# Kernel optimization log

Measured on AMD Instinct MI355X. Metric: run time of the kernel, lower is better.

Reference implementation:

```python
import jax, jax.numpy as jnp
import numpy as np

C, H, D = 64, 2, 32
NQ, NA, NE, F_IN = 8192, 32768, 500000, 128
E_E2Q, E_E2E, E_E2A, E_Q2A = 131072, 800000, 262144, 32768
N_POS, N_NEG = 8192, 24576
# node types: 0=question, 1=answer, 2=entity
# edge types (src_type, dst_type): e2q=(2,0), e2e=(2,2), e2a=(2,1), q2a=(0,1)
REL_ST = [(2, 0), (2, 2), (2, 1), (0, 1)]


def _edges(k, n_src, n_dst, e):
    k1, k2 = jax.random.split(k)
    return jnp.stack([jax.random.randint(k1, (e,), 0, n_src),
                      jax.random.randint(k2, (e,), 0, n_dst)]).astype(jnp.int32)


def setup_inputs():
    key = jax.random.key(0)
    ks = jax.random.split(key, 16)
    inp = {
        'x_question': jax.random.normal(ks[0], (NQ, F_IN), jnp.float32),
        'x_answer': jax.random.normal(ks[1], (NA, F_IN), jnp.float32),
        'x_entity': jax.random.normal(ks[2], (NE, F_IN), jnp.float32),
        'e_e2q': _edges(ks[3], NE, NQ, E_E2Q),
        'e_e2e': _edges(ks[4], NE, NE, E_E2E),
        'e_e2a': _edges(ks[5], NE, NA, E_E2A),
        'e_q2a': _edges(ks[6], NQ, NA, E_Q2A),
        'pos_idx': _edges(ks[7], NQ, NA, N_POS),
        'neg_idx': _edges(ks[8], NQ, NA, N_NEG),
        # learned parameters (stacked over the 3 node types / 4 edge types)
        'W_in': jax.random.normal(ks[9], (3, F_IN, C), jnp.float32) / np.sqrt(F_IN).astype(np.float32),
        'b_in': jnp.zeros((3, C), jnp.float32),
        'bn_gamma': jnp.ones((3, C), jnp.float32),
        'bn_beta': jnp.zeros((3, C), jnp.float32),
        'W_kqv': jax.random.normal(ks[10], (3, C, 3 * C), jnp.float32) / np.sqrt(C).astype(np.float32),
        'b_kqv': jnp.zeros((3, 3 * C), jnp.float32),
        'A_k': jax.random.normal(ks[11], (4, H, D, D), jnp.float32) / np.sqrt(D).astype(np.float32),
        'A_v': jax.random.normal(ks[12], (4, H, D, D), jnp.float32) / np.sqrt(D).astype(np.float32),
        'p_rel': jnp.ones((4, H), jnp.float32),
        'W_out': jax.random.normal(ks[13], (3, C, C), jnp.float32) / np.sqrt(C).astype(np.float32),
        'b_out': jnp.zeros((3, C), jnp.float32),
        'skip': jnp.ones((3,), jnp.float32),
    }
    return inp


def _segment_attn(scores, vals, dst, n):
    # scores [E,H], vals [E,H,D]: softmax over incoming edges per dst node, weighted scatter-add
    m = jax.ops.segment_max(scores, dst, num_segments=n)          # [N,H]
    e = jnp.exp(scores - m[dst])                                   # [E,H]
    s = jax.ops.segment_sum(e, dst, num_segments=n)                # [N,H]
    w = e / s[dst]
    return jax.ops.segment_sum(vals * w[..., None], dst, num_segments=n)  # [N,H,D]


def _forward(x_question, x_answer, x_entity, W_in, b_in, bn_gamma, bn_beta,
             W_kqv, b_kqv, A_k, A_v, p_rel, W_out, b_out, skip, edges):
    xs = [x_question, x_answer, x_entity]
    h = []
    for t in range(3):
        y = jax.nn.relu(xs[t] @ W_in[t] + b_in[t])
        mu = y.mean(0)
        var = y.var(0)  # biased, as in torch BN training mode
        y = bn_gamma[t] * (y - mu) * jax.lax.rsqrt(var + 1e-5) + bn_beta[t]
        h.append(y)
    kqv = [h[t] @ W_kqv[t] + b_kqv[t] for t in range(3)]
    k = [kv[:, :C].reshape(-1, H, D) for kv in kqv]
    q = [kv[:, C:2 * C].reshape(-1, H, D) for kv in kqv]
    v = [kv[:, 2 * C:].reshape(-1, H, D) for kv in kqv]
    by_dst = {0: [], 1: [], 2: []}
    inv_sqrt_d = jnp.float32(1.0 / np.sqrt(D))
    for r, ((st, dt), ei) in enumerate(zip(REL_ST, edges)):
        src, dst = ei[0], ei[1]
        k_r = jnp.einsum('ehd,hdf->ehf', k[st][src], A_k[r])   # per-relation key transform
        v_r = jnp.einsum('ehd,hdf->ehf', v[st][src], A_v[r])   # per-relation value transform
        sc = (q[dt][dst] * k_r).sum(-1) * p_rel[r] * inv_sqrt_d  # [E,H]
        by_dst[dt].append((sc, v_r, dst))
    out = []
    for t in range(3):
        sc = jnp.concatenate([a for a, _, _ in by_dst[t]], axis=0)
        vr = jnp.concatenate([b for _, b, _ in by_dst[t]], axis=0)
        dst = jnp.concatenate([c for _, _, c in by_dst[t]], axis=0)
        n = h[t].shape[0]
        agg = _segment_attn(sc, vr, dst, n).reshape(n, C)
        a = jax.nn.gelu(agg, approximate=False) @ W_out[t] + b_out[t]
        g = jax.nn.sigmoid(skip[t])
        out.append(g * a + (1.0 - g) * h[t])
    return out  # [z_question, z_answer, z_entity]


def reference(x_question, x_answer, x_entity, e_e2q, e_e2e, e_e2a, e_q2a,
              pos_idx, neg_idx, W_in, b_in, bn_gamma, bn_beta, W_kqv, b_kqv,
              A_k, A_v, p_rel, W_out, b_out, skip):
    zq, za, ze = _forward(x_question, x_answer, x_entity, W_in, b_in, bn_gamma,
                          bn_beta, W_kqv, b_kqv, A_k, A_v, p_rel, W_out, b_out,
                          skip, [e_e2q, e_e2e, e_e2a, e_q2a])
    pos_pred = (zq[pos_idx[0]] * za[pos_idx[1]]).sum(-1)
    neg_pred = (zq[neg_idx[0]] * za[neg_idx[1]]).sum(-1)
    return pos_pred, neg_pred, zq, za, ze
```

## Files before the change

kernel.cpp:

```cpp
#include <hip/hip_runtime.h>
#include <hip/hip_bf16.h>
#include <hip/hip_fp16.h>
#include <math.h>

#define NQ 8192
#define NA 32768
#define NE 500000
#define F_IN 128
#define E_E2Q 131072
#define E_E2E 800000
#define E_E2A 262144
#define E_Q2A 32768
#define N_POS 8192
#define N_NEG 24576

#define NT_TOTAL (NQ + NA + NE)
#define E_TOTAL (E_E2Q + E_E2E + E_E2A + E_Q2A)
#define NBLK_SCAN ((NT_TOTAL + 1023) / 1024)
#define CDIV(a, b) (((a) + (b) - 1) / (b))

#define BASE_Q 0
#define BASE_A NQ
#define BASE_E (NQ + NA)

#define GIN_Q 128
#define GIN_A 512
#define GIN_E 768

#define GB_Q 2048
#define GB_E 4096
#define GB_A 8192

#define TOP_Q 64
#define TOP_A 256
#define TOP_E 3907

typedef _Float16 half8_t __attribute__((ext_vector_type(8)));
typedef _Float16 half4_t __attribute__((ext_vector_type(4)));
typedef _Float16 half2_t __attribute__((ext_vector_type(2)));
typedef float f32x4_t __attribute__((ext_vector_type(4)));

__device__ inline void load_lds16(const void* g, void* l) {
  __builtin_amdgcn_global_load_lds((const __attribute__((address_space(1))) void*)g,
                                   (__attribute__((address_space(3))) void*)l, 16, 0, 0);
}

__device__ inline float fast_gelu(float v) {
  float u = 1.5957691216057308f * fmaf(0.044715f * v * v, v, v);
  return v / (1.f + __expf(-u));
}


__global__ __launch_bounds__(256) void prep_misc(
    float* __restrict__ row_start_f,
    const float* __restrict__ W_in, _Float16* __restrict__ WinT,
    const float* __restrict__ W_out, _Float16* __restrict__ WoutT)
{
  int bid = blockIdx.x;
  if (bid < 128) {
    size_t i = (size_t)bid * 256 + threadIdx.x;
    size_t stride = (size_t)128 * 256;
    for (; i < NT_TOTAL; i += stride) row_start_f[i] = 0.f;
  } else if (bid < 320) {
    int b = bid - 128;
    int t = b >> 6, n = b & 63, k = threadIdx.x;
    if (k < 136) {
      float v = (k < 128) ? W_in[(size_t)t * 128 * 64 + (size_t)k * 64 + n] : 0.f;
      WinT[((size_t)t * 64 + n) * 136 + k] = (_Float16)v;
    }
  } else {
    int b = bid - 320;
    int t = b >> 6, n = b & 63, k = threadIdx.x;
    if (k < 72) {
      float v = (k < 64) ? W_out[(size_t)t * 64 * 64 + (size_t)k * 64 + n] : 0.f;
      WoutT[((size_t)t * 64 + n) * 72 + k] = (_Float16)v;
    }
  }
}


__global__ __launch_bounds__(256) void gemm_inproj_all(
    const float* __restrict__ xq, const float* __restrict__ xa,
    const float* __restrict__ xe,
    const _Float16* __restrict__ WinT, const float* __restrict__ b_in,
    _Float16* __restrict__ y_h, float* __restrict__ bstats)
{
  __shared__ __align__(16) float bufA[32 * 128];
  __shared__ __align__(16) float bufB[32 * 128];
  __shared__ _Float16 Bs[64 * 136];
  __shared__ float s1[64], s2[64];

  int bid = blockIdx.x;
  int t, lb, nb;
  const float* Af;
  _Float16* oh;
  if (bid < GIN_Q)              { t = 0; lb = bid;                 nb = GIN_Q; Af = xq; oh = y_h; }
  else if (bid < GIN_Q + GIN_A) { t = 1; lb = bid - GIN_Q;         nb = GIN_A; Af = xa; oh = y_h + (size_t)NQ * 64; }
  else                          { t = 2; lb = bid - GIN_Q - GIN_A; nb = GIN_E; Af = xe; oh = y_h + (size_t)(NQ + NA) * 64; }
  int M = (t == 0) ? NQ : (t == 1) ? NA : NE;
  int nh = CDIV(M, 32);
  const _Float16* WT = WinT + (size_t)t * 64 * 136;
  const float* bias = b_in + t * 64;

  int tid = threadIdx.x, w = tid >> 6, l = tid & 63;
  int lr = l & 15, lg = l >> 4;
  int wrow = (w & 1) * 16;
  int wcol = (w >> 1) * 32;

  for (int idx = tid; idx < 64 * 136 / 8; idx += 256)
    *(half8_t*)&Bs[idx * 8] = *(const half8_t*)&WT[(size_t)idx * 8];
  if (tid < 64) { s1[tid] = 0.f; s2[tid] = 0.f; }

  float bval[2];
  bval[0] = bias[wcol + lr];
  bval[1] = bias[wcol + 16 + lr];
// ... 58 lines not shown
        oh[(size_t)row * 64 + col] = (_Float16)val;
        ps1[ct] += val;
        ps2[ct] += val * val;
      }
    }
    __builtin_amdgcn_s_barrier();
    float* tmp = cur; cur = nxt; nxt = tmp;
  }

#pragma unroll
  for (int ct = 0; ct < 2; ++ct) {
    int col = wcol + ct * 16 + lr;
    atomicAdd(&s1[col], ps1[ct]);
    atomicAdd(&s2[col], ps2[ct]);
  }
  __syncthreads();
  if (tid < 64) {
    bstats[(size_t)blockIdx.x * 128 + tid] = s1[tid];
    bstats[(size_t)blockIdx.x * 128 + 64 + tid] = s2[tid];
  }
}


__global__ __launch_bounds__(256) void gemm_out_all(
    const _Float16* __restrict__ agg_h, const _Float16* __restrict__ y_h,
    const _Float16* __restrict__ WoutT, const float* __restrict__ b_out,
    const float* __restrict__ scale, const float* __restrict__ shift,
    const float* __restrict__ skip, float* __restrict__ zout)
{
  __shared__ _Float16 Bs[64 * 72];
  int bid = blockIdx.x;
  int t, row0, M;
  size_t nodeoff;
  if (bid < TOP_Q)              { t = 0; row0 = bid * 128;              M = NQ; nodeoff = 0; }
  else if (bid < TOP_Q + TOP_A) { t = 1; row0 = (bid - TOP_Q) * 128;    M = NA; nodeoff = NQ; }
  else                          { t = 2; row0 = (bid - TOP_Q - TOP_A) * 128; M = NE; nodeoff = NQ + NA; }
  const _Float16* Ah = agg_h + nodeoff * 64;
  const _Float16* resh = y_h + nodeoff * 64;
  float* Cf = zout + nodeoff * 64;
  const _Float16* WT = WoutT + (size_t)t * 64 * 72;
  const float* bias = b_out + t * 64;
  const float* rsc = scale + t * 64;
  const float* rsh = shift + t * 64;

  int tid = threadIdx.x;
  int w = tid >> 6, l = tid & 63;
  int lr = l & 15, lg = l >> 4;

  for (int idx = tid; idx < 64 * 72 / 8; idx += 256)
    *(half8_t*)&Bs[idx * 8] = *(const half8_t*)&WT[(size_t)idx * 8];

  half8_t afrag[2][2];
#pragma unroll
  for (int rt = 0; rt < 2; ++rt) {
    int gr = row0 + w * 32 + rt * 16 + lr;
    bool ok = gr < M;
#pragma unroll
    for (int ks = 0; ks < 2; ++ks) {
      half8_t h8 = {};
      if (ok) h8 = *(const half8_t*)&Ah[(size_t)gr * 64 + ks * 32 + lg * 8];
      afrag[rt][ks] = h8;
    }
  }
  __syncthreads();

  f32x4_t acc[2][4] = {};
#pragma unroll
  for (int ks = 0; ks < 2; ++ks) {
#pragma unroll
    for (int ct = 0; ct < 4; ++ct) {
      half8_t b = *(const half8_t*)&Bs[(ct * 16 + lr) * 72 + ks * 32 + lg * 8];
      acc[0][ct] = __builtin_amdgcn_mfma_f32_16x16x32_f16(afrag[0][ks], b, acc[0][ct], 0, 0, 0);
      acc[1][ct] = __builtin_amdgcn_mfma_f32_16x16x32_f16(afrag[1][ks], b, acc[1][ct], 0, 0, 0);
    }
  }

  float g = 1.f / (1.f + __expf(-skip[t]));
  float gb = 1.f - g;
#pragma unroll
  for (int rt = 0; rt < 2; ++rt) {
    int rbase = row0 + w * 32 + rt * 16 + lg * 4;
#pragma unroll
    for (int ct = 0; ct < 4; ++ct) {
      int col = ct * 16 + lr;
      float bval = bias[col];
#pragma unroll
      for (int j = 0; j < 4; ++j) {
        int row = rbase + j;
        if (row >= M) continue;
        float val = acc[rt][ct][j] + bval;
        float rv = (float)resh[(size_t)row * 64 + col];
        Cf[(size_t)row * 64 + col] = g * val + gb * (rsc[col] * rv + rsh[col]);
      }
    }
  }
}


template <int BM, int BNT, int KTOT>
__global__ __launch_bounds__(BM * 2) void gemm_mfma(
    const _Float16* __restrict__ Ah,
    const _Float16* __restrict__ WT, const float* __restrict__ bias, int M,
    _Float16* __restrict__ oh, int LDO)
{
  constexpr int KP = KTOT + 8;
  constexpr int NTHR = BM * 2;
  constexpr int TP = BNT + 8;
  constexpr int SZ_AB = (BM * KP + BNT * KP) * 2;
  constexpr int SZ_T = 128 * TP * 2;
  constexpr int SZ = SZ_AB > SZ_T ? SZ_AB : SZ_T;
  __shared__ __align__(16) char smem[SZ];
  _Float16* As = (_Float16*)smem;
  _Float16* Bs = As + BM * KP;
  _Float16* Ts = (_Float16*)smem;
  int tid = threadIdx.x;
  int row0 = blockIdx.x * BM;
  int colbase = blockIdx.y * BNT;

  {
    constexpr int CH = KTOT / 8;
    for (int idx = tid; idx < BM * CH; idx += NTHR) {
      int row = idx / CH, c = idx % CH;
      int gr = row0 + row;
      half8_t a8 = {};
      if (gr < M) a8 = *(const half8_t*)&Ah[(size_t)gr * KTOT + c * 8];
      *(half8_t*)&As[row * KP + c * 8] = a8;
    }
  }
  {
    const _Float16* wsrc = WT + (size_t)colbase * KP;
    for (int idx = tid; idx < BNT * KP / 8; idx += NTHR)
      *(half8_t*)&Bs[idx * 8] = *(const half8_t*)&wsrc[(size_t)idx * 8];
  }
  __syncthreads();

  int w = tid >> 6, l = tid & 63;
  int lr = l & 15, lg = l >> 4;
  constexpr int NCT = BNT / 16;
  constexpr int NKS = KTOT / 32;
  f32x4_t acc[2][NCT] = {};
#pragma unroll
  for (int ks = 0; ks < NKS; ++ks) {
    half8_t a0 = *(const half8_t*)&As[(w * 32 + lr) * KP + ks * 32 + lg * 8];
    half8_t a1 = *(const half8_t*)&As[(w * 32 + 16 + lr) * KP + ks * 32 + lg * 8];
#pragma unroll
    for (int ct = 0; ct < NCT; ++ct) {
      half8_t b = *(const half8_t*)&Bs[(ct * 16 + lr) * KP + ks * 32 + lg * 8];
      acc[0][ct] = __builtin_amdgcn_mfma_f32_16x16x32_f16(a0, b, acc[0][ct], 0, 0, 0);
      acc[1][ct] = __builtin_amdgcn_mfma_f32_16x16x32_f16(a1, b, acc[1][ct], 0, 0, 0);
    }
  }

  float bval[NCT];
#pragma unroll
  for (int ct = 0; ct < NCT; ++ct) bval[ct] = bias[colbase + ct * 16 + lr];

#pragma unroll
  for (int rt = 0; rt < 2; ++rt) {
    __syncthreads();
    int r2base = w * 16 + lg * 4;
#pragma unroll
    for (int ct = 0; ct < NCT; ++ct) {
      int colL = ct * 16 + lr;
#pragma unroll
      for (int j = 0; j < 4; ++j)
        Ts[(r2base + j) * TP + colL] = (_Float16)(acc[rt][ct][j] + bval[ct]);
    }
    __syncthreads();
    constexpr int C8 = BNT / 8;
    for (int idx = tid; idx < 128 * C8; idx += NTHR) {
      int r2 = idx / C8, c8 = (idx % C8) * 8;
      int gr = row0 + (r2 >> 4) * 32 + rt * 16 + (r2 & 15);
      if (gr < M)
        *(half8_t*)&oh[(size_t)gr * LDO + colbase + c8] = *(const half8_t*)&Ts[r2 * TP + c8];
    }
  }
}


__global__ __launch_bounds__(256) void stats_reduce(const float* __restrict__ bstats,
                                                    float* __restrict__ stats) {
  __shared__ float sh[256];
  int t = blockIdx.x >> 7;
  int c = blockIdx.x & 127;
  int nb = (t == 0) ? GIN_Q : (t == 1) ? GIN_A : GIN_E;
  int base = (t == 0) ? 0 : (t == 1) ? GIN_Q : (GIN_Q + GIN_A);
  float s = 0.f;
  for (int i = threadIdx.x; i < nb; i += 256)
    s += bstats[(size_t)(base + i) * 128 + c];
  sh[threadIdx.x] = s;
  __syncthreads();
  for (int off2 = 128; off2 > 0; off2 >>= 1) {
    if (threadIdx.x < off2) sh[threadIdx.x] += sh[threadIdx.x + off2];
    __syncthreads();
  }
  if (threadIdx.x == 0) stats[t * 128 + c] = sh[0];
}

__global__ void bn_finalize(const float* __restrict__ stats,
                            const float* __restrict__ gamma, const float* __restrict__ beta,
                            float* __restrict__ scale, float* __restrict__ shift) {
  int t = threadIdx.x;
  if (t >= 192) return;
  int ty = t >> 6, c = t & 63;
  float invN = (ty == 0) ? (1.f / NQ) : (ty == 1) ? (1.f / NA) : (1.f / NE);
  float mu = stats[ty * 128 + c] * invN;
  float var = stats[ty * 128 + 64 + c] * invN - mu * mu;
  float rs = rsqrtf(var + 1e-5f);
  float gm = gamma[ty * 64 + c];
  scale[t] = gm * rs;
  shift[t] = beta[ty * 64 + c] - gm * mu * rs;
}

__global__ void kqv_bias2(const float* __restrict__ b_kqv, const float* __restrict__ W_kqv,
                          const float* __restrict__ shift, float* __restrict__ bias2) {
  int t = blockIdx.x, n = threadIdx.x;
  float s = b_kqv[t * 192 + n];
  for (int k = 0; k < 64; ++k)
    s += shift[t * 64 + k] * W_kqv[(size_t)t * 64 * 192 + k * 192 + n];
  bias2[t * 192 + n] = s;
}


__global__ void wprep_kqv(const float* __restrict__ W_kqv, const float* __restrict__ bias2,
                          const float* __restrict__ A_k, const float* __restrict__ A_v,
                          const float* __restrict__ scale,
                          _Float16* __restrict__ WqT, _Float16* __restrict__ WeT,
                          _Float16* __restrict__ WaT, float* __restrict__ bias_big) {
  int j = blockIdx.x;
  int c = threadIdx.x;
  int t, jj, bofs;
  _Float16* W;
  if (j < 192)      { t = 0; jj = j;       W = WqT; bofs = 0; }
  else if (j < 512) { t = 2; jj = j - 192; W = WeT; bofs = 192; }
  else              { t = 1; jj = j - 512; W = WaT; bofs = 512; }
  const float* Wt = W_kqv + (size_t)t * 64 * 192;
  const float* b2 = bias2 + t * 192;
  int mode = 0, rel = 0, sub = 0;
  if (t == 1) { mode = 1; rel = (jj < 64) ? 2 : 3; sub = jj & 63; }
  else if (jj >= 64 && jj < 128) { mode = 1; rel = (t == 0) ? 0 : 1; sub = jj - 64; }
  else if (jj >= 128) {
    mode = 2; sub = (jj - 128) & 63;
    rel = (t == 0) ? 3 : ((jj - 128) >> 6);
  }
  int h = sub >> 5, x = sub & 31;
  float wv, bv;
  if (mode == 0) {
    wv = Wt[(size_t)c * 192 + jj];
    bv = b2[jj];
  } else if (mode == 1) {
    const float* Ar = A_k + ((size_t)rel * 2048 + h * 1024 + x * 32);
    float s = 0.f, sb = 0.f;
    for (int f = 0; f < 32; ++f) {
      float a = Ar[f];
      s = fmaf(a, Wt[(size_t)c * 192 + 64 + h * 32 + f], s);
      sb = fmaf(a, b2[64 + h * 32 + f], sb);
    }
    wv = s; bv = sb;
  } else {
    const float* Ar = A_v + ((size_t)rel * 2048 + h * 1024 + x);
    float s = 0.f, sb = 0.f;
    for (int d = 0; d < 32; ++d) {
      float a = Ar[d * 32];
      s = fmaf(a, Wt[(size_t)c * 192 + 128 + h * 32 + d], s);
      sb = fmaf(a, b2[128 + h * 32 + d], sb);
    }
    wv = s; bv = sb;
  }
  wv *= scale[t * 64 + c];
  W[(size_t)jj * 72 + c] = (_Float16)wv;
  if (c < 8) W[(size_t)jj * 72 + 64 + c] = (_Float16)0.f;
  if (c == 0) bias_big[bofs + jj] = bv;
}


__global__ __launch_bounds__(256) void hist_all(
    const int* __restrict__ d0, const int* __restrict__ d1,
    const int* __restrict__ d2, const int* __restrict__ d3,
    unsigned* __restrict__ cnt)
{
  int i = blockIdx.x * blockDim.x + threadIdx.x;
  int stride = gridDim.x * blockDim.x;
  for (; i < E_TOTAL; i += stride) {
    if (i < E_E2Q) atomicAdd(&cnt[BASE_Q + d0[i]], 1u);
    else if (i < E_E2Q + E_E2E) atomicAdd(&cnt[BASE_E + d1[i - E_E2Q]], 1u);
    else if (i < E_E2Q + E_E2E + E_E2A) atomicAdd(&cnt[BASE_A + d2[i - E_E2Q - E_E2E]], 1u);
    else atomicAdd(&cnt[BASE_A + d3[i - E_E2Q - E_E2E - E_E2A]], 1u);
  }
}

__global__ __launch_bounds__(256) void scan1(unsigned* __restrict__ arr, int n,
                                             unsigned* __restrict__ bsums) {
  __shared__ unsigned sh[256];
  int t = threadIdx.x;
  int base = blockIdx.x * 1024 + t * 4;
  unsigned v[4];
  unsigned s = 0;
#pragma unroll
  for (int j = 0; j < 4; ++j) {
    v[j] = (base + j < n) ? arr[base + j] : 0u;
    s += v[j];
  }
  sh[t] = s;
  __syncthreads();
  for (int off = 1; off < 256; off <<= 1) {
    unsigned x = (t >= off) ? sh[t - off] : 0u;
    __syncthreads();
    sh[t] += x;
    __syncthreads();
  }
  unsigned run = sh[t] - s;
#pragma unroll
  for (int j = 0; j < 4; ++j) {
    if (base + j < n) arr[base + j] = run;
    run += v[j];
  }
  if (t == 255) bsums[blockIdx.x] = sh[255];
}

__global__ __launch_bounds__(256) void scan2(unsigned* __restrict__ bsums, int nb) {
  __shared__ unsigned sh[256];
  __shared__ unsigned carry;
  int t = threadIdx.x;
  if (t == 0) carry = 0;
  __syncthreads();
  for (int chunk = 0; chunk < nb; chunk += 256) {
    int i = chunk + t;
    unsigned v = (i < nb) ? bsums[i] : 0u;
    sh[t] = v;
    __syncthreads();
    for (int off = 1; off < 256; off <<= 1) {
      unsigned x = (t >= off) ? sh[t - off] : 0u;
      __syncthreads();
      sh[t] += x;
      __syncthreads();
    }
    unsigned inc = sh[t];
    unsigned c = carry;
    __syncthreads();
    if (i < nb) bsums[i] = c + inc - v;
    if (t == 255) carry = c + sh[255];
    __syncthreads();
  }
}

__global__ __launch_bounds__(256) void scan3(unsigned* __restrict__ arr,
                                             const unsigned* __restrict__ bsums,
                                             unsigned* __restrict__ cursor, int n) {
  int t = threadIdx.x;
  int base = blockIdx.x * 1024 + t * 4;
  unsigned add = bsums[blockIdx.x];
#pragma unroll
  for (int j = 0; j < 4; ++j) {
    int idx = base + j;
    if (idx < n) {
      unsigned r = arr[idx] + add;
      arr[idx] = r;
      cursor[idx] = r;
    }
  }
}

__global__ __launch_bounds__(256) void scatter_all(
    const int* __restrict__ s0, const int* __restrict__ d0,
    const int* __restrict__ s1, const int* __restrict__ d1,
    const int* __restrict__ s2, const int* __restrict__ d2,
    const int* __restrict__ s3, const int* __restrict__ d3,
    unsigned* __restrict__ cursor, unsigned* __restrict__ eidx)
{
  int i = blockIdx.x * blockDim.x + threadIdx.x;
  int stride = gridDim.x * blockDim.x;
  for (; i < E_TOTAL; i += stride) {
    unsigned pos, pay;
    if (i < E_E2Q) {
      pos = atomicAdd(&cursor[BASE_Q + d0[i]], 1u);
      pay = (unsigned)(s0[i] * 320);
    } else if (i < E_E2Q + E_E2E) {
      int k = i - E_E2Q;
      pos = atomicAdd(&cursor[BASE_E + d1[k]], 1u);
      pay = (unsigned)(s1[k] * 320);
    } else if (i < E_E2Q + E_E2E + E_E2A) {
      int k = i - E_E2Q - E_E2E;
      pos = atomicAdd(&cursor[BASE_A + d2[k]], 1u);
      pay = (unsigned)(s2[k] * 320);
    } else {
      int k = i - E_E2Q - E_E2E - E_E2A;
      pos = atomicAdd(&cursor[BASE_A + d3[k]], 1u);
      pay = (unsigned)(s3[k] * 192) | 0x80000000u;
    }
    eidx[pos] = pay;
  }
}


template <int NREL>
__device__ __forceinline__ void gather_body(
    int bidLocal, int nblocks, int N, int nodebase,
    const unsigned* __restrict__ row_start, const unsigned* __restrict__ row_end,
    const unsigned* __restrict__ eidx,
    const _Float16* __restrict__ baseA, int vofA,
    const _Float16* __restrict__ baseB, int vofB,
    const _Float16* __restrict__ qtA, int ldqA,
    const _Float16* __restrict__ qtB, int ldqB,
    const float* __restrict__ prelA, const float* __restrict__ prelB,
    _Float16* __restrict__ agg)
{
  int lane = threadIdx.x & 63;
  int h = lane >> 5, f = lane & 31;
  int idx2 = h * 32 + 2 * (f & 15);
  const float isd = 0.17677669529663687f;
  float pr0 = prelA[h] * isd;
  float pr1 = (NREL == 2) ? prelB[h] * isd : 0.f;

// ... 91 lines not shown
  }
}

__global__ __launch_bounds__(256) void gather_all(
    const unsigned* __restrict__ row_start, const unsigned* __restrict__ row_end,
    const unsigned* __restrict__ eidx,
    const _Float16* __restrict__ kqvQ, const _Float16* __restrict__ kqvE,
    const _Float16* __restrict__ kqvA,
    const float* __restrict__ p_rel, _Float16* __restrict__ agg)
{
  int bid = blockIdx.x;
  if (bid < GB_Q) {
    gather_body<1>(bid, GB_Q, NQ, BASE_Q, row_start, row_end, eidx,
                   kqvE, 128, kqvE, 128, kqvQ + 64, 192, kqvQ + 64, 192,
                   p_rel + 0, p_rel + 0, agg);
  } else if (bid < GB_Q + GB_E) {
    gather_body<1>(bid - GB_Q, GB_E, NE, BASE_E, row_start, row_end, eidx,
                   kqvE, 192, kqvE, 192, kqvE + 64, 320, kqvE + 64, 320,
                   p_rel + 2, p_rel + 2, agg);
  } else {
    gather_body<2>(bid - GB_Q - GB_E, GB_A, NA, BASE_A, row_start, row_end, eidx,
                   kqvE, 256, kqvQ, 128, kqvA, 128, kqvA + 64, 128,
                   p_rel + 4, p_rel + 6, agg);
  }
}


__global__ void pred_all(const int* __restrict__ pos, const int* __restrict__ neg,
                         const float* __restrict__ zq, const float* __restrict__ za,
                         float* __restrict__ outp) {
  int i = blockIdx.x * blockDim.x + threadIdx.x;
  if (i >= N_POS + N_NEG) return;
  int k; const int* qi; const int* ai; float* o;
  if (i < N_POS) { k = i; qi = pos; ai = pos + N_POS; o = outp; }
  else { k = i - N_POS; qi = neg; ai = neg + N_NEG; o = outp + N_POS; }
  const float4* a = (const float4*)(zq + (size_t)qi[k] * 64);
  const float4* b = (const float4*)(za + (size_t)ai[k] * 64);
  float ssum = 0.f;
#pragma unroll
  for (int j = 0; j < 16; ++j) {
    float4 x = a[j], y = b[j];
    ssum += x.x * y.x + x.y * y.y + x.z * y.z + x.w * y.w;
  }
  o[k] = ssum;
}

// ... 21 lines not shown
  const float* p_rel = (const float*)d_in[17];
  const float* W_out = (const float*)d_in[18];
  const float* b_out = (const float*)d_in[19];
  const float* skip = (const float*)d_in[20];
  float* out = (float*)d_out;

  float* ws = (float*)d_ws;
  size_t off = 0;
  _Float16* y_h = (_Float16*)(ws + off);    off += (size_t)NT_TOTAL * 32;
  _Float16* kqvQ = (_Float16*)(ws + off);   off += (size_t)NQ * 96;
  _Float16* kqvE = (_Float16*)(ws + off);   off += (size_t)NE * 160;
  _Float16* kqvA = (_Float16*)(ws + off);   off += (size_t)NA * 64;
  _Float16* agg_h = (_Float16*)(ws + off);  off += (size_t)NT_TOTAL * 32;
  float* stats = ws + off;                  off += 384;
  float* scale = ws + off;                  off += 192;
  float* shift = ws + off;                  off += 192;
  float* bias2 = ws + off;                  off += 576;
  float* bias_big = ws + off;               off += 640;
  _Float16* WqT = (_Float16*)(ws + off);    off += 192 * 72 / 2;
  _Float16* WeT = (_Float16*)(ws + off);    off += 320 * 72 / 2;
  _Float16* WaT = (_Float16*)(ws + off);    off += 128 * 72 / 2;
  _Float16* WinT = (_Float16*)(ws + off);   off += 3 * 64 * 136 / 2;
  _Float16* WoutT = (_Float16*)(ws + off);  off += 3 * 64 * 72 / 2;
  float* bstats = ws + off;                 off += (size_t)(GIN_Q + GIN_A + GIN_E) * 128;
  unsigned* row_start = (unsigned*)(ws + off); off += NT_TOTAL;
  unsigned* cursor = (unsigned*)(ws + off);    off += NT_TOTAL;
  unsigned* bsums = (unsigned*)(ws + off);     off += 1024;
  unsigned* eidx = (unsigned*)(ws + off);      off += E_TOTAL + 8;

  float* zq_out = out + (N_POS + N_NEG);

  prep_misc<<<dim3(512), dim3(256), 0, stream>>>((float*)row_start, W_in, WinT, W_out, WoutT);

  gemm_inproj_all<<<dim3(GIN_Q + GIN_A + GIN_E), dim3(256), 0, stream>>>(
      xq, xa, xe, WinT, b_in, y_h, bstats);

  stats_reduce<<<dim3(384), dim3(256), 0, stream>>>(bstats, stats);
  bn_finalize<<<dim3(1), dim3(192), 0, stream>>>(stats, bn_gamma, bn_beta, scale, shift);
  kqv_bias2<<<dim3(3), dim3(192), 0, stream>>>(b_kqv, W_kqv, shift, bias2);
  wprep_kqv<<<dim3(640), dim3(64), 0, stream>>>(W_kqv, bias2, A_k, A_v, scale,
                                                WqT, WeT, WaT, bias_big);

  gemm_mfma<256, 192, 64><<<dim3(CDIV(NQ, 256)), dim3(512), 0, stream>>>(
      y_h, WqT, bias_big, NQ, kqvQ, 192);
  gemm_mfma<256, 160, 64><<<dim3(CDIV(NE, 256), 2), dim3(512), 0, stream>>>(
      y_h + (size_t)(NQ + NA) * 64, WeT, bias_big + 192, NE, kqvE, 320);
  gemm_mfma<256, 128, 64><<<dim3(CDIV(NA, 256)), dim3(512), 0, stream>>>(
      y_h + (size_t)NQ * 64, WaT, bias_big + 512, NA, kqvA, 128);

  hist_all<<<dim3(2048), dim3(256), 0, stream>>>(
      e_e2q + E_E2Q, e_e2e + E_E2E, e_e2a + E_E2A, e_q2a + E_Q2A, row_start);
  scan1<<<dim3(NBLK_SCAN), dim3(256), 0, stream>>>(row_start, NT_TOTAL, bsums);
  scan2<<<dim3(1), dim3(256), 0, stream>>>(bsums, NBLK_SCAN);
  scan3<<<dim3(NBLK_SCAN), dim3(256), 0, stream>>>(row_start, bsums, cursor, NT_TOTAL);
  scatter_all<<<dim3(2048), dim3(256), 0, stream>>>(
      e_e2q, e_e2q + E_E2Q, e_e2e, e_e2e + E_E2E,
      e_e2a, e_e2a + E_E2A, e_q2a, e_q2a + E_Q2A, cursor, eidx);

  gather_all<<<dim3(GB_Q + GB_E + GB_A), dim3(256), 0, stream>>>(
      row_start, cursor, eidx, kqvQ, kqvE, kqvA, p_rel, agg_h);

  gemm_out_all<<<dim3(TOP_Q + TOP_A + TOP_E), dim3(256), 0, stream>>>(
      agg_h, y_h, WoutT, b_out, scale, shift, skip, zq_out);

  pred_all<<<dim3(CDIV(N_POS + N_NEG, 256)), dim3(256), 0, stream>>>(
      pos_idx, neg_idx, zq_out, zq_out + (size_t)NQ * 64, out);
}
```

Before: 709.7 us.

## Merge independent launches into horizontally fused kernels to cut launch count

Horizontally fuses independent stages into shared launches, with block ranges selecting the work. The edge histogram rides with the input projection, the BN stats reduction with scan1, BN finalize and bias2 with scan2, and weight prep with scan3. The three KQV GEMMs and the CSR scatter now share one launch with dynamic shared memory. This removes many small launches and serial gaps so that graph-building work overlaps the dense GEMMs. In exchange, the fused kernels carry a larger shared-memory footprint and 512-thread blocks for the scatter part, which may lower occupancy.

New measurement: 655.1 us. 1.08x faster.

```diff
diff --git a/kernel.cpp b/kernel.cpp
--- a/kernel.cpp
+++ b/kernel.cpp
@@ -26,6 +26,8 @@
 #define GIN_Q 128
 #define GIN_A 512
 #define GIN_E 768
+#define GIN_TOT (GIN_Q + GIN_A + GIN_E)
+#define HB 1024
 
 #define GB_Q 2048
 #define GB_E 4096
@@ -35,8 +37,14 @@
 #define TOP_A 256
 #define TOP_E 3907
 
+#define KQ_Q 32
+#define KQ_E 1954
+#define KQ_A 128
+#define KQ_TOT (KQ_Q + 2 * KQ_E + KQ_A)
+#define SCB 2048
+#define SMEM_KQV 64512
+
 typedef _Float16 half8_t __attribute__((ext_vector_type(8)));
-typedef _Float16 half4_t __attribute__((ext_vector_type(4)));
 typedef _Float16 half2_t __attribute__((ext_vector_type(2)));
 typedef float f32x4_t __attribute__((ext_vector_type(4)));
 
@@ -79,11 +87,14 @@
 }
 
 
-__global__ __launch_bounds__(256) void gemm_inproj_all(
+__global__ __launch_bounds__(256) void inproj_hist_all(
     const float* __restrict__ xq, const float* __restrict__ xa,
     const float* __restrict__ xe,
     const _Float16* __restrict__ WinT, const float* __restrict__ b_in,
-    _Float16* __restrict__ y_h, float* __restrict__ bstats)
+    _Float16* __restrict__ y_h, float* __restrict__ bstats,
+    const int* __restrict__ hd0, const int* __restrict__ hd1,
+    const int* __restrict__ hd2, const int* __restrict__ hd3,
+    unsigned* __restrict__ cnt)
 {
   __shared__ __align__(16) float bufA[32 * 128];
   __shared__ __align__(16) float bufB[32 * 128];
@@ -91,6 +102,19 @@
   __shared__ float s1[64], s2[64];
 
   int bid = blockIdx.x;
+  if (bid >= GIN_TOT) {
+    int i = (bid - GIN_TOT) * 256 + threadIdx.x;
+    int stride = HB * 256;
+    for (; i < E_TOTAL; i += stride) {
+      if (i < E_E2Q) atomicAdd(&cnt[BASE_Q + hd0[i]], 1u);
+      else if (i < E_E2Q + E_E2E) atomicAdd(&cnt[BASE_E + hd1[i - E_E2Q]], 1u);
+      else if (i < E_E2Q + E_E2E + E_E2A)
+        atomicAdd(&cnt[BASE_A + hd2[i - E_E2Q - E_E2E]], 1u);
+      else atomicAdd(&cnt[BASE_A + hd3[i - E_E2Q - E_E2E - E_E2A]], 1u);
+    }
+    return;
+  }
+
   int t, lb, nb;
   const float* Af;
   _Float16* oh;
@@ -195,213 +219,145 @@
 }
 
 
-__global__ __launch_bounds__(256) void gemm_out_all(
-    const _Float16* __restrict__ agg_h, const _Float16* __restrict__ y_h,
-    const _Float16* __restrict__ WoutT, const float* __restrict__ b_out,
-    const float* __restrict__ scale, const float* __restrict__ shift,
-    const float* __restrict__ skip, float* __restrict__ zout)
-{
-  __shared__ _Float16 Bs[64 * 72];
+__global__ __launch_bounds__(256) void reduce_scan1(
+    const float* __restrict__ bstats, float* __restrict__ stats,
+    unsigned* __restrict__ arr, unsigned* __restrict__ bsums)
+{
+  __shared__ __align__(16) char shbuf[1024];
   int bid = blockIdx.x;
-  int t, row0, M;
-  size_t nodeoff;
-  if (bid < TOP_Q)              { t = 0; row0 = bid * 128;              M = NQ; nodeoff = 0; }
-  else if (bid < TOP_Q + TOP_A) { t = 1; row0 = (bid - TOP_Q) * 128;    M = NA; nodeoff = NQ; }
-  else                          { t = 2; row0 = (bid - TOP_Q - TOP_A) * 128; M = NE; nodeoff = NQ + NA; }
-  const _Float16* Ah = agg_h + nodeoff * 64;
-  const _Float16* resh = y_h + nodeoff * 64;
-  float* Cf = zout + nodeoff * 64;
-  const _Float16* WT = WoutT + (size_t)t * 64 * 72;
-  const float* bias = b_out + t * 64;
-  const float* rsc = scale + t * 64;
-  const float* rsh = shift + t * 64;
-
-  int tid = threadIdx.x;
-  int w = tid >> 6, l = tid & 63;
-  int lr = l & 15, lg = l >> 4;
-
-  for (int idx = tid; idx < 64 * 72 / 8; idx += 256)
-    *(half8_t*)&Bs[idx * 8] = *(const half8_t*)&WT[(size_t)idx * 8];
-
-  half8_t afrag[2][2];
-#pragma unroll
-  for (int rt = 0; rt < 2; ++rt) {
-    int gr = row0 + w * 32 + rt * 16 + lr;
-    bool ok = gr < M;
-#pragma unroll
-    for (int ks = 0; ks < 2; ++ks) {
-      half8_t h8 = {};
-      if (ok) h8 = *(const half8_t*)&Ah[(size_t)gr * 64 + ks * 32 + lg * 8];
-      afrag[rt][ks] = h8;
-    }
-  }
-  __syncthreads();
-
-  f32x4_t acc[2][4] = {};
-#pragma unroll
-  for (int ks = 0; ks < 2; ++ks) {
-#pragma unroll
-    for (int ct = 0; ct < 4; ++ct) {
-      half8_t b = *(const half8_t*)&Bs[(ct * 16 + lr) * 72 + ks * 32 + lg * 8];
-      acc[0][ct] = __builtin_amdgcn_mfma_f32_16x16x32_f16(afrag[0][ks], b, acc[0][ct], 0, 0, 0);
-      acc[1][ct] = __builtin_amdgcn_mfma_f32_16x16x32_f16(afrag[1][ks], b, acc[1][ct], 0, 0, 0);
-    }
-  }
-
-  float g = 1.f / (1.f + __expf(-skip[t]));
-  float gb = 1.f - g;
-#pragma unroll
-  for (int rt = 0; rt < 2; ++rt) {
-    int rbase = row0 + w * 32 + rt * 16 + lg * 4;
-#pragma unroll
-    for (int ct = 0; ct < 4; ++ct) {
-      int col = ct * 16 + lr;
-      float bval = bias[col];
-#pragma unroll
-      for (int j = 0; j < 4; ++j) {
-        int row = rbase + j;
-        if (row >= M) continue;
-        float val = acc[rt][ct][j] + bval;
-        float rv = (float)resh[(size_t)row * 64 + col];
-        Cf[(size_t)row * 64 + col] = g * val + gb * (rsc[col] * rv + rsh[col]);
+  int t0 = threadIdx.x;
+  if (bid < 384) {
+    float* sh = (float*)shbuf;
+    int t = bid >> 7, c = bid & 127;
+    int nb = (t == 0) ? GIN_Q : (t == 1) ? GIN_A : GIN_E;
+    int base = (t == 0) ? 0 : (t == 1) ? GIN_Q : (GIN_Q + GIN_A);
+    float s = 0.f;
+    for (int i = t0; i < nb; i += 256)
+      s += bstats[(size_t)(base + i) * 128 + c];
+    sh[t0] = s;
+    __syncthreads();
+    for (int off2 = 128; off2 > 0; off2 >>= 1) {
+      if (t0 < off2) sh[t0] += sh[t0 + off2];
+      __syncthreads();
+    }
+    if (t0 == 0) stats[t * 128 + c] = sh[0];
+  } else {
+    unsigned* sh = (unsigned*)shbuf;
+    int blk = bid - 384;
+    int base = blk * 1024 + t0 * 4;
+    unsigned v[4];
+    unsigned s = 0;
+#pragma unroll
+    for (int j = 0; j < 4; ++j) {
+      v[j] = (base + j < NT_TOTAL) ? arr[base + j] : 0u;
+      s += v[j];
+    }
+    sh[t0] = s;
+    __syncthreads();
+    for (int off = 1; off < 256; off <<= 1) {
+      unsigned x = (t0 >= off) ? sh[t0 - off] : 0u;
+      __syncthreads();
+      sh[t0] += x;
+      __syncthreads();
+    }
+    unsigned run = sh[t0] - s;
+#pragma unroll
+    for (int j = 0; j < 4; ++j) {
+      if (base + j < NT_TOTAL) arr[base + j] = run;
+      run += v[j];
+    }
+    if (t0 == 255) bsums[blk] = sh[255];
+  }
+}
+
+
+__global__ __launch_bounds__(256) void scan2_bn(
+    unsigned* __restrict__ bsums, int nbk,
+    const float* __restrict__ stats,
+    const float* __restrict__ gamma, const float* __restrict__ beta,
+    float* __restrict__ scale, float* __restrict__ shift,
+    const float* __restrict__ b_kqv, const float* __restrict__ W_kqv,
+    float* __restrict__ bias2)
+{
+  int t0 = threadIdx.x;
+  if (blockIdx.x == 0) {
+    __shared__ unsigned sh[256];
+    __shared__ unsigned carry;
+    if (t0 == 0) carry = 0;
+    __syncthreads();
+    for (int chunk = 0; chunk < nbk; chunk += 256) {
+      int i = chunk + t0;
+      unsigned v = (i < nbk) ? bsums[i] : 0u;
+      sh[t0] = v;
+      __syncthreads();
+      for (int off = 1; off < 256; off <<= 1) {
+        unsigned x = (t0 >= off) ? sh[t0 - off] : 0u;
+        __syncthreads();
+        sh[t0] += x;
+        __syncthreads();
       }
-    }
-  }
-}
-
-
-template <int BM, int BNT, int KTOT>
-__global__ __launch_bounds__(BM * 2) void gemm_mfma(
-    const _Float16* __restrict__ Ah,
-    const _Float16* __restrict__ WT, const float* __restrict__ bias, int M,
-    _Float16* __restrict__ oh, int LDO)
-{
-  constexpr int KP = KTOT + 8;
-  constexpr int NTHR = BM * 2;
-  constexpr int TP = BNT + 8;
-  constexpr int SZ_AB = (BM * KP + BNT * KP) * 2;
-  constexpr int SZ_T = 128 * TP * 2;
-  constexpr int SZ = SZ_AB > SZ_T ? SZ_AB : SZ_T;
-  __shared__ __align__(16) char smem[SZ];
-  _Float16* As = (_Float16*)smem;
-  _Float16* Bs = As + BM * KP;
-  _Float16* Ts = (_Float16*)smem;
-  int tid = threadIdx.x;
-  int row0 = blockIdx.x * BM;
-  int colbase = blockIdx.y * BNT;
-
-  {
-    constexpr int CH = KTOT / 8;
-    for (int idx = tid; idx < BM * CH; idx += NTHR) {
-      int row = idx / CH, c = idx % CH;
-      int gr = row0 + row;
-      half8_t a8 = {};
-      if (gr < M) a8 = *(const half8_t*)&Ah[(size_t)gr * KTOT + c * 8];
-      *(half8_t*)&As[row * KP + c * 8] = a8;
-    }
-  }
-  {
-    const _Float16* wsrc = WT + (size_t)colbase * KP;
-    for (int idx = tid; idx < BNT * KP / 8; idx += NTHR)
-      *(half8_t*)&Bs[idx * 8] = *(const half8_t*)&wsrc[(size_t)idx * 8];
-  }
-  __syncthreads();
-
-  int w = tid >> 6, l = tid & 63;
-  int lr = l & 15, lg = l >> 4;
-  constexpr int NCT = BNT / 16;
-  constexpr int NKS = KTOT / 32;
-  f32x4_t acc[2][NCT] = {};
-#pragma unroll
-  for (int ks = 0; ks < NKS; ++ks) {
-    half8_t a0 = *(const half8_t*)&As[(w * 32 + lr) * KP + ks * 32 + lg * 8];
-    half8_t a1 = *(const half8_t*)&As[(w * 32 + 16 + lr) * KP + ks * 32 + lg * 8];
-#pragma unroll
-    for (int ct = 0; ct < NCT; ++ct) {
-      half8_t b = *(const half8_t*)&Bs[(ct * 16 + lr) * KP + ks * 32 + lg * 8];
-      acc[0][ct] = __builtin_amdgcn_mfma_f32_16x16x32_f16(a0, b, acc[0][ct], 0, 0, 0);
-      acc[1][ct] = __builtin_amdgcn_mfma_f32_16x16x32_f16(a1, b, acc[1][ct], 0, 0, 0);
-    }
-  }
-
-  float bval[NCT];
-#pragma unroll
-  for (int ct = 0; ct < NCT; ++ct) bval[ct] = bias[colbase + ct * 16 + lr];
-
-#pragma unroll
-  for (int rt = 0; rt < 2; ++rt) {
+      unsigned inc = sh[t0];
+      unsigned c = carry;
+      __syncthreads();
+      if (i < nbk) bsums[i] = c + inc - v;
+      if (t0 == 255) carry = c + sh[255];
+      __syncthreads();
+    }
+  } else {
+    __shared__ float sshift[192];
+    if (t0 < 192) {
+      int ty = t0 >> 6, c = t0 & 63;
+      float invN = (ty == 0) ? (1.f / NQ) : (ty == 1) ? (1.f / NA) : (1.f / NE);
+      float mu = stats[ty * 128 + c] * invN;
+      float var = stats[ty * 128 + 64 + c] * invN - mu * mu;
+      float rs = rsqrtf(var + 1e-5f);
+      float gm = gamma[t0];
+      float sc = gm * rs;
+      float sf = beta[t0] - gm * mu * rs;
+      scale[t0] = sc;
+      shift[t0] = sf;
+      sshift[t0] = sf;
+    }
     __syncthreads();
-    int r2base = w * 16 + lg * 4;
-#pragma unroll
-    for (int ct = 0; ct < NCT; ++ct) {
-      int colL = ct * 16 + lr;
-#pragma unroll
-      for (int j = 0; j < 4; ++j)
-        Ts[(r2base + j) * TP + colL] = (_Float16)(acc[rt][ct][j] + bval[ct]);
-    }
-    __syncthreads();
-    constexpr int C8 = BNT / 8;
-    for (int idx = tid; idx < 128 * C8; idx += NTHR) {
-      int r2 = idx / C8, c8 = (idx % C8) * 8;
-      int gr = row0 + (r2 >> 4) * 32 + rt * 16 + (r2 & 15);
-      if (gr < M)
-        *(half8_t*)&oh[(size_t)gr * LDO + colbase + c8] = *(const half8_t*)&Ts[r2 * TP + c8];
-    }
-  }
-}
-
-
-__global__ __launch_bounds__(256) void stats_reduce(const float* __restrict__ bstats,
-                                                    float* __restrict__ stats) {
-  __shared__ float sh[256];
-  int t = blockIdx.x >> 7;
-  int c = blockIdx.x & 127;
-  int nb = (t == 0) ? GIN_Q : (t == 1) ? GIN_A : GIN_E;
-  int base = (t == 0) ? 0 : (t == 1) ? GIN_Q : (GIN_Q + GIN_A);
-  float s = 0.f;
-  for (int i = threadIdx.x; i < nb; i += 256)
-    s += bstats[(size_t)(base + i) * 128 + c];
-  sh[threadIdx.x] = s;
-  __syncthreads();
-  for (int off2 = 128; off2 > 0; off2 >>= 1) {
-    if (threadIdx.x < off2) sh[threadIdx.x] += sh[threadIdx.x + off2];
-    __syncthreads();
-  }
-  if (threadIdx.x == 0) stats[t * 128 + c] = sh[0];
-}
-
-__global__ void bn_finalize(const float* __restrict__ stats,
-                            const float* __restrict__ gamma, const float* __restrict__ beta,
-                            float* __restrict__ scale, float* __restrict__ shift) {
-  int t = threadIdx.x;
-  if (t >= 192) return;
-  int ty = t >> 6, c = t & 63;
-  float invN = (ty == 0) ? (1.f / NQ) : (ty == 1) ? (1.f / NA) : (1.f / NE);
-  float mu = stats[ty * 128 + c] * invN;
-  float var = stats[ty * 128 + 64 + c] * invN - mu * mu;
-  float rs = rsqrtf(var + 1e-5f);
-  float gm = gamma[ty * 64 + c];
-  scale[t] = gm * rs;
-  shift[t] = beta[ty * 64 + c] - gm * mu * rs;
-}
-
-__global__ void kqv_bias2(const float* __restrict__ b_kqv, const float* __restrict__ W_kqv,
-                          const float* __restrict__ shift, float* __restrict__ bias2) {
-  int t = blockIdx.x, n = threadIdx.x;
-  float s = b_kqv[t * 192 + n];
-  for (int k = 0; k < 64; ++k)
-    s += shift[t * 64 + k] * W_kqv[(size_t)t * 64 * 192 + k * 192 + n];
-  bias2[t * 192 + n] = s;
-}
-
-
-__global__ void wprep_kqv(const float* __restrict__ W_kqv, const float* __restrict__ bias2,
-                          const float* __restrict__ A_k, const float* __restrict__ A_v,
-                          const float* __restrict__ scale,
-                          _Float16* __restrict__ WqT, _Float16* __restrict__ WeT,
-                          _Float16* __restrict__ WaT, float* __restrict__ bias_big) {
-  int j = blockIdx.x;
-  int c = threadIdx.x;
+    for (int idx = t0; idx < 576; idx += 256) {
+      int t = idx / 192, n = idx % 192;
+      float s = b_kqv[t * 192 + n];
+      for (int k = 0; k < 64; ++k)
+        s += sshift[t * 64 + k] * W_kqv[(size_t)t * 64 * 192 + k * 192 + n];
+      bias2[t * 192 + n] = s;
+    }
+  }
+}
+
+
+__global__ __launch_bounds__(256) void scan3_wprep(
+    unsigned* __restrict__ arr, const unsigned* __restrict__ bsums,
+    unsigned* __restrict__ cursor,
+    const float* __restrict__ W_kqv, const float* __restrict__ bias2,
+    const float* __restrict__ A_k, const float* __restrict__ A_v,
+    const float* __restrict__ scale,
+    _Float16* __restrict__ WqT, _Float16* __restrict__ WeT,
+    _Float16* __restrict__ WaT, float* __restrict__ bias_big)
+{
+  int bid = blockIdx.x;
+  int t0 = threadIdx.x;
+  if (bid < NBLK_SCAN) {
+    int base = bid * 1024 + t0 * 4;
+    unsigned add = bsums[bid];
+#pragma unroll
+    for (int j = 0; j < 4; ++j) {
+      int idx = base + j;
+      if (idx < NT_TOTAL) {
+        unsigned r = arr[idx] + add;
+        arr[idx] = r;
+        cursor[idx] = r;
+      }
+    }
+    return;
+  }
+  int j = (bid - NBLK_SCAN) * 4 + (t0 >> 6);
+  int c = t0 & 63;
+  if (j >= 640) return;
   int t, jj, bofs;
   _Float16* W;
   if (j < 192)      { t = 0; jj = j;       W = WqT; bofs = 0; }
@@ -447,121 +403,128 @@
 }
 
 
-__global__ __launch_bounds__(256) void hist_all(
-    const int* __restrict__ d0, const int* __restrict__ d1,
-    const int* __restrict__ d2, const int* __restrict__ d3,
-    unsigned* __restrict__ cnt)
-{
-  int i = blockIdx.x * blockDim.x + threadIdx.x;
-  int stride = gridDim.x * blockDim.x;
-  for (; i < E_TOTAL; i += stride) {
-    if (i < E_E2Q) atomicAdd(&cnt[BASE_Q + d0[i]], 1u);
-    else if (i < E_E2Q + E_E2E) atomicAdd(&cnt[BASE_E + d1[i - E_E2Q]], 1u);
-    else if (i < E_E2Q + E_E2E + E_E2A) atomicAdd(&cnt[BASE_A + d2[i - E_E2Q - E_E2E]], 1u);
-    else atomicAdd(&cnt[BASE_A + d3[i - E_E2Q - E_E2E - E_E2A]], 1u);
-  }
-}
-
-__global__ __launch_bounds__(256) void scan1(unsigned* __restrict__ arr, int n,
-                                             unsigned* __restrict__ bsums) {
-  __shared__ unsigned sh[256];
-  int t = threadIdx.x;
-  int base = blockIdx.x * 1024 + t * 4;
-  unsigned v[4];
-  unsigned s = 0;
-#pragma unroll
-  for (int j = 0; j < 4; ++j) {
-    v[j] = (base + j < n) ? arr[base + j] : 0u;
-    s += v[j];
-  }
-  sh[t] = s;
+template <int BNT>
+__device__ __forceinline__ void kqv_body(
+    char* smem,
+    const _Float16* __restrict__ Ah,
+    const _Float16* __restrict__ WT, const float* __restrict__ bias, int M,
+    _Float16* __restrict__ oh, int LDO, int row0, int colbase)
+{
+  constexpr int KP = 72;
+  constexpr int TP = BNT + 8;
+  _Float16* As = (_Float16*)smem;
+  _Float16* Bs = As + 256 * KP;
+  _Float16* Ts = (_Float16*)smem;
+  int tid = threadIdx.x;
+
+  {
+    for (int idx = tid; idx < 256 * 8; idx += 512) {
+      int row = idx >> 3, c = (idx & 7);
+      int gr = row0 + row;
+      half8_t a8 = {};
+      if (gr < M) a8 = *(const half8_t*)&Ah[(size_t)gr * 64 + c * 8];
+      *(half8_t*)&As[row * KP + c * 8] = a8;
+    }
+  }
+  {
+    const _Float16* wsrc = WT + (size_t)colbase * KP;
+    for (int idx = tid; idx < BNT * KP / 8; idx += 512)
+      *(half8_t*)&Bs[idx * 8] = *(const half8_t*)&wsrc[(size_t)idx * 8];
+  }
   __syncthreads();
-  for (int off = 1; off < 256; off <<= 1) {
-    unsigned x = (t >= off) ? sh[t - off] : 0u;
+
+  int w = tid >> 6, l = tid & 63;
+  int lr = l & 15, lg = l >> 4;
+  constexpr int NCT = BNT / 16;
+  f32x4_t acc[2][NCT] = {};
+#pragma unroll
+  for (int ks = 0; ks < 2; ++ks) {
+    half8_t a0 = *(const half8_t*)&As[(w * 32 + lr) * KP + ks * 32 + lg * 8];
+    half8_t a1 = *(const half8_t*)&As[(w * 32 + 16 + lr) * KP + ks * 32 + lg * 8];
+#pragma unroll
+    for (int ct = 0; ct < NCT; ++ct) {
+      half8_t b = *(const half8_t*)&Bs[(ct * 16 + lr) * KP + ks * 32 + lg * 8];
+      acc[0][ct] = __builtin_amdgcn_mfma_f32_16x16x32_f16(a0, b, acc[0][ct], 0, 0, 0);
+      acc[1][ct] = __builtin_amdgcn_mfma_f32_16x16x32_f16(a1, b, acc[1][ct], 0, 0, 0);
+    }
+  }
+
+  float bval[NCT];
+#pragma unroll
+  for (int ct = 0; ct < NCT; ++ct) bval[ct] = bias[colbase + ct * 16 + lr];
+
+#pragma unroll
+  for (int rt = 0; rt < 2; ++rt) {
     __syncthreads();
-    sh[t] += x;
+    int r2base = w * 16 + lg * 4;
+#pragma unroll
+    for (int ct = 0; ct < NCT; ++ct) {
+      int colL = ct * 16 + lr;
+#pragma unroll
+      for (int j = 0; j < 4; ++j)
+        Ts[(r2base + j) * TP + colL] = (_Float16)(acc[rt][ct][j] + bval[ct]);
+    }
     __syncthreads();
-  }
-  unsigned run = sh[t] - s;
-#pragma unroll
-  for (int j = 0; j < 4; ++j) {
-    if (base + j < n) arr[base + j] = run;
-    run += v[j];
-  }
-  if (t == 255) bsums[blockIdx.x] = sh[255];
-}
-
-__global__ __launch_bounds__(256) void scan2(unsigned* __restrict__ bsums, int nb) {
-  __shared__ unsigned sh[256];
-  __shared__ unsigned carry;
-  int t = threadIdx.x;
-  if (t == 0) carry = 0;
-  __syncthreads();
-  for (int chunk = 0; chunk < nb; chunk += 256) {
-    int i = chunk + t;
-    unsigned v = (i < nb) ? bsums[i] : 0u;
-    sh[t] = v;
-    __syncthreads();
-    for (int off = 1; off < 256; off <<= 1) {
-      unsigned x = (t >= off) ? sh[t - off] : 0u;
-      __syncthreads();
-      sh[t] += x;
-      __syncthreads();
-    }
-    unsigned inc = sh[t];
-    unsigned c = carry;
-    __syncthreads();
-    if (i < nb) bsums[i] = c + inc - v;
-    if (t == 255) carry = c + sh[255];
-    __syncthreads();
-  }
-}
-
-__global__ __launch_bounds__(256) void scan3(unsigned* __restrict__ arr,
-                                             const unsigned* __restrict__ bsums,
-                                             unsigned* __restrict__ cursor, int n) {
-  int t = threadIdx.x;
-  int base = blockIdx.x * 1024 + t * 4;
-  unsigned add = bsums[blockIdx.x];
-#pragma unroll
-  for (int j = 0; j < 4; ++j) {
-    int idx = base + j;
-    if (idx < n) {
-      unsigned r = arr[idx] + add;
-      arr[idx] = r;
-      cursor[idx] = r;
-    }
-  }
-}
-
-__global__ __launch_bounds__(256) void scatter_all(
+    constexpr int C8 = BNT / 8;
+    for (int idx = tid; idx < 128 * C8; idx += 512) {
+      int r2 = idx / C8, c8 = (idx % C8) * 8;
+      int gr = row0 + (r2 >> 4) * 32 + rt * 16 + (r2 & 15);
+      if (gr < M)
+        *(half8_t*)&oh[(size_t)gr * LDO + colbase + c8] = *(const half8_t*)&Ts[r2 * TP + c8];
+    }
+  }
+}
+
+
+__global__ __launch_bounds__(512) void kqv_scatter(
+    const _Float16* __restrict__ y_h,
+    const _Float16* __restrict__ WqT, const _Float16* __restrict__ WeT,
+    const _Float16* __restrict__ WaT, const float* __restrict__ bias_big,
+    _Float16* __restrict__ kqvQ, _Float16* __restrict__ kqvE,
+    _Float16* __restrict__ kqvA,
     const int* __restrict__ s0, const int* __restrict__ d0,
     const int* __restrict__ s1, const int* __restrict__ d1,
     const int* __restrict__ s2, const int* __restrict__ d2,
     const int* __restrict__ s3, const int* __restrict__ d3,
     unsigned* __restrict__ cursor, unsigned* __restrict__ eidx)
 {
-  int i = blockIdx.x * blockDim.x + threadIdx.x;
-  int stride = gridDim.x * blockDim.x;
-  for (; i < E_TOTAL; i += stride) {
-    unsigned pos, pay;
-    if (i < E_E2Q) {
-      pos = atomicAdd(&cursor[BASE_Q + d0[i]], 1u);
-      pay = (unsigned)(s0[i] * 320);
-    } else if (i < E_E2Q + E_E2E) {
-      int k = i - E_E2Q;
-      pos = atomicAdd(&cursor[BASE_E + d1[k]], 1u);
-      pay = (unsigned)(s1[k] * 320);
-    } else if (i < E_E2Q + E_E2E + E_E2A) {
-      int k = i - E_E2Q - E_E2E;
-      pos = atomicAdd(&cursor[BASE_A + d2[k]], 1u);
-      pay = (unsigned)(s2[k] * 320);
-    } else {
-      int k = i - E_E2Q - E_E2E - E_E2A;
-      pos = atomicAdd(&cursor[BASE_A + d3[k]], 1u);
-      pay = (unsigned)(s3[k] * 192) | 0x80000000u;
-    }
-    eidx[pos] = pay;
+  extern __shared__ __align__(16) char smem[];
+  int bid = blockIdx.x;
+  if (bid < KQ_Q) {
+    kqv_body<192>(smem, y_h, WqT, bias_big, NQ, kqvQ, 192, bid * 256, 0);
+  } else if (bid < KQ_Q + 2 * KQ_E) {
+    int b = bid - KQ_Q;
+    int ct = b / KQ_E;
+    int rb = b % KQ_E;
+    kqv_body<160>(smem, y_h + (size_t)(NQ + NA) * 64, WeT, bias_big + 192, NE,
+                  kqvE, 320, rb * 256, ct * 160);
+  } else if (bid < KQ_TOT) {
+    int b = bid - KQ_Q - 2 * KQ_E;
+    kqv_body<128>(smem, y_h + (size_t)NQ * 64, WaT, bias_big + 512, NA,
+                  kqvA, 128, b * 256, 0);
+  } else {
+    int i = (bid - KQ_TOT) * 512 + threadIdx.x;
+    int stride = SCB * 512;
+    for (; i < E_TOTAL; i += stride) {
+      unsigned pos, pay;
+      if (i < E_E2Q) {
+        pos = atomicAdd(&cursor[BASE_Q + d0[i]], 1u);
+        pay = (unsigned)(s0[i] * 320);
+      } else if (i < E_E2Q + E_E2E) {
+        int k = i - E_E2Q;
+        pos = atomicAdd(&cursor[BASE_E + d1[k]], 1u);
+        pay = (unsigned)(s1[k] * 320);
+      } else if (i < E_E2Q + E_E2E + E_E2A) {
+        int k = i - E_E2Q - E_E2E;
+        pos = atomicAdd(&cursor[BASE_A + d2[k]], 1u);
+        pay = (unsigned)(s2[k] * 320);
+      } else {
+        int k = i - E_E2Q - E_E2E - E_E2A;
+        pos = atomicAdd(&cursor[BASE_A + d3[k]], 1u);
+        pay = (unsigned)(s3[k] * 192) | 0x80000000u;
+      }
+      eidx[pos] = pay;
+    }
   }
 }
 
@@ -699,6 +662,81 @@
     gather_body<2>(bid - GB_Q - GB_E, GB_A, NA, BASE_A, row_start, row_end, eidx,
                    kqvE, 256, kqvQ, 128, kqvA, 128, kqvA + 64, 128,
                    p_rel + 4, p_rel + 6, agg);
+  }
+}
+
+
+__global__ __launch_bounds__(256) void gemm_out_all(
+    const _Float16* __restrict__ agg_h, const _Float16* __restrict__ y_h,
+    const _Float16* __restrict__ WoutT, const float* __restrict__ b_out,
+    const float* __restrict__ scale, const float* __restrict__ shift,
+    const float* __restrict__ skip, float* __restrict__ zout)
+{
+  __shared__ _Float16 Bs[64 * 72];
+  int bid = blockIdx.x;
+  int t, row0, M;
+  size_t nodeoff;
+  if (bid < TOP_Q)              { t = 0; row0 = bid * 128;              M = NQ; nodeoff = 0; }
+  else if (bid < TOP_Q + TOP_A) { t = 1; row0 = (bid - TOP_Q) * 128;    M = NA; nodeoff = NQ; }
+  else                          { t = 2; row0 = (bid - TOP_Q - TOP_A) * 128; M = NE; nodeoff = NQ + NA; }
+  const _Float16* Ah = agg_h + nodeoff * 64;
+  const _Float16* resh = y_h + nodeoff * 64;
+  float* Cf = zout + nodeoff * 64;
+  const _Float16* WT = WoutT + (size_t)t * 64 * 72;
+  const float* bias = b_out + t * 64;
+  const float* rsc = scale + t * 64;
+  const float* rsh = shift + t * 64;
+
+  int tid = threadIdx.x;
+  int w = tid >> 6, l = tid & 63;
+  int lr = l & 15, lg = l >> 4;
+
+  for (int idx = tid; idx < 64 * 72 / 8; idx += 256)
+    *(half8_t*)&Bs[idx * 8] = *(const half8_t*)&WT[(size_t)idx * 8];
+
+  half8_t afrag[2][2];
+#pragma unroll
+  for (int rt = 0; rt < 2; ++rt) {
+    int gr = row0 + w * 32 + rt * 16 + lr;
+    bool ok = gr < M;
+#pragma unroll
+    for (int ks = 0; ks < 2; ++ks) {
+      half8_t h8 = {};
+      if (ok) h8 = *(const half8_t*)&Ah[(size_t)gr * 64 + ks * 32 + lg * 8];
+      afrag[rt][ks] = h8;
+    }
+  }
+  __syncthreads();
+
+  f32x4_t acc[2][4] = {};
+#pragma unroll
+  for (int ks = 0; ks < 2; ++ks) {
+#pragma unroll
+    for (int ct = 0; ct < 4; ++ct) {
+      half8_t b = *(const half8_t*)&Bs[(ct * 16 + lr) * 72 + ks * 32 + lg * 8];
+      acc[0][ct] = __builtin_amdgcn_mfma_f32_16x16x32_f16(afrag[0][ks], b, acc[0][ct], 0, 0, 0);
+      acc[1][ct] = __builtin_amdgcn_mfma_f32_16x16x32_f16(afrag[1][ks], b, acc[1][ct], 0, 0, 0);
+    }
+  }
+
+  float g = 1.f / (1.f + __expf(-skip[t]));
+  float gb = 1.f - g;
+#pragma unroll
+  for (int rt = 0; rt < 2; ++rt) {
+    int rbase = row0 + w * 32 + rt * 16 + lg * 4;
+#pragma unroll
+    for (int ct = 0; ct < 4; ++ct) {
+      int col = ct * 16 + lr;
+      float bval = bias[col];
+#pragma unroll
+      for (int j = 0; j < 4; ++j) {
+        int row = rbase + j;
+        if (row >= M) continue;
+        float val = acc[rt][ct][j] + bval;
+        float rv = (float)resh[(size_t)row * 64 + col];
+        Cf[(size_t)row * 64 + col] = g * val + gb * (rsc[col] * rv + rsh[col]);
+      }
+    }
   }
 }
 
@@ -766,7 +804,7 @@
   _Float16* WaT = (_Float16*)(ws + off);    off += 128 * 72 / 2;
   _Float16* WinT = (_Float16*)(ws + off);   off += 3 * 64 * 136 / 2;
   _Float16* WoutT = (_Float16*)(ws + off);  off += 3 * 64 * 72 / 2;
-  float* bstats = ws + off;                 off += (size_t)(GIN_Q + GIN_A + GIN_E) * 128;
+  float* bstats = ws + off;                 off += (size_t)GIN_TOT * 128;
   unsigned* row_start = (unsigned*)(ws + off); off += NT_TOTAL;
   unsigned* cursor = (unsigned*)(ws + off);    off += NT_TOTAL;
   unsigned* bsums = (unsigned*)(ws + off);     off += 1024;
@@ -776,28 +814,22 @@
 
   prep_misc<<<dim3(512), dim3(256), 0, stream>>>((float*)row_start, W_in, WinT, W_out, WoutT);
 
-  gemm_inproj_all<<<dim3(GIN_Q + GIN_A + GIN_E), dim3(256), 0, stream>>>(
-      xq, xa, xe, WinT, b_in, y_h, bstats);
-
-  stats_reduce<<<dim3(384), dim3(256), 0, stream>>>(bstats, stats);
-  bn_finalize<<<dim3(1), dim3(192), 0, stream>>>(stats, bn_gamma, bn_beta, scale, shift);
-  kqv_bias2<<<dim3(3), dim3(192), 0, stream>>>(b_kqv, W_kqv, shift, bias2);
-  wprep_kqv<<<dim3(640), dim3(64), 0, stream>>>(W_kqv, bias2, A_k, A_v, scale,
-                                                WqT, WeT, WaT, bias_big);
-
-  gemm_mfma<256, 192, 64><<<dim3(CDIV(NQ, 256)), dim3(512), 0, stream>>>(
-      y_h, WqT, bias_big, NQ, kqvQ, 192);
-  gemm_mfma<256, 160, 64><<<dim3(CDIV(NE, 256), 2), dim3(512), 0, stream>>>(
-      y_h + (size_t)(NQ + NA) * 64, WeT, bias_big + 192, NE, kqvE, 320);
-  gemm_mfma<256, 128, 64><<<dim3(CDIV(NA, 256)), dim3(512), 0, stream>>>(
-      y_h + (size_t)NQ * 64, WaT, bias_big + 512, NA, kqvA, 128);
-
-  hist_all<<<dim3(2048), dim3(256), 0, stream>>>(
+  inproj_hist_all<<<dim3(GIN_TOT + HB), dim3(256), 0, stream>>>(
+      xq, xa, xe, WinT, b_in, y_h, bstats,
       e_e2q + E_E2Q, e_e2e + E_E2E, e_e2a + E_E2A, e_q2a + E_Q2A, row_start);
-  scan1<<<dim3(NBLK_SCAN), dim3(256), 0, stream>>>(row_start, NT_TOTAL, bsums);
-  scan2<<<dim3(1), dim3(256), 0, stream>>>(bsums, NBLK_SCAN);
-  scan3<<<dim3(NBLK_SCAN), dim3(256), 0, stream>>>(row_start, bsums, cursor, NT_TOTAL);
-  scatter_all<<<dim3(2048), dim3(256), 0, stream>>>(
+
+  reduce_scan1<<<dim3(384 + NBLK_SCAN), dim3(256), 0, stream>>>(
+      bstats, stats, row_start, bsums);
+
+  scan2_bn<<<dim3(2), dim3(256), 0, stream>>>(
+      bsums, NBLK_SCAN, stats, bn_gamma, bn_beta, scale, shift, b_kqv, W_kqv, bias2);
+
+  scan3_wprep<<<dim3(NBLK_SCAN + 160), dim3(256), 0, stream>>>(
+      row_start, bsums, cursor, W_kqv, bias2, A_k, A_v, scale,
+      WqT, WeT, WaT, bias_big);
+
+  kqv_scatter<<<dim3(KQ_TOT + SCB), dim3(512), SMEM_KQV, stream>>>(
+      y_h, WqT, WeT, WaT, bias_big, kqvQ, kqvE, kqvA,
       e_e2q, e_e2q + E_E2Q, e_e2e, e_e2e + E_E2E,
       e_e2a, e_e2a + E_E2A, e_q2a, e_q2a + E_Q2A, cursor, eidx);
 
```
